# Performance work log

Measured on AMD Instinct MI355X. Metric: run time of the kernel, lower is better.

## Reference

```python
import jax, jax.numpy as jnp
import numpy as np

HIDDEN = 1024
N_HEAD = 16
HEAD_DIM = HIDDEN // N_HEAD
ROPE_THETA = 10000.0


def setup_inputs() -> dict:
    key = jax.random.key(0)
    ks = jax.random.split(key, 6)
    B, T = 4, 2048
    x = jax.random.normal(ks[0], (B, T, HIDDEN), dtype=jnp.float32)
    rnn_state = jax.random.normal(ks[1], (B, HIDDEN), dtype=jnp.float32)
    Wqkv = jax.random.normal(ks[2], (HIDDEN, 3 * HIDDEN), dtype=jnp.float32) * 0.02
    bqkv = jnp.zeros((3 * HIDDEN,), dtype=jnp.float32)
    Wproj = jax.random.normal(ks[3], (HIDDEN, HIDDEN), dtype=jnp.float32) * 0.02
    bproj = jnp.zeros((HIDDEN,), dtype=jnp.float32)
    return {"x": x, "rnn_state": rnn_state, "Wqkv": Wqkv, "bqkv": bqkv,
            "Wproj": Wproj, "bproj": bproj}


def _rope_tables(T, dtype):
    # GPT-NeoX style half-split RoPE
    inv_freq = 1.0 / (ROPE_THETA ** (jnp.arange(0, HEAD_DIM, 2, dtype=jnp.float32) / HEAD_DIM))
    freqs = jnp.arange(T, dtype=jnp.float32)[:, None] * inv_freq[None, :]  # [T, D/2]
    return jnp.cos(freqs).astype(dtype), jnp.sin(freqs).astype(dtype)


def _apply_rope(x, cos, sin):
    # x: [B, H, T, D]; cos/sin: [T, D/2]
    x1, x2 = jnp.split(x, 2, axis=-1)
    c = cos[None, None, :, :]
    s = sin[None, None, :, :]
    return jnp.concatenate([x1 * c - x2 * s, x1 * s + x2 * c], axis=-1)


def reference(x, rnn_state, Wqkv, bqkv, Wproj, bproj):
    B, T, C = x.shape
    qkv = x @ Wqkv + bqkv  # [B, T, 3C]
    q, k, v = jnp.split(qkv, 3, axis=-1)
    # split heads -> [B, H, T, D]
    def heads(t):
        return t.reshape(B, T, N_HEAD, HEAD_DIM).transpose(0, 2, 1, 3)
    q, k, v = heads(q), heads(k), heads(v)
    cos, sin = _rope_tables(T, x.dtype)
    q = _apply_rope(q, cos, sin)
    k = _apply_rope(k, cos, sin)
    scale = 1.0 / jnp.sqrt(jnp.asarray(HEAD_DIM, dtype=x.dtype))
    scores = jnp.einsum('bhtd,bhsd->bhts', q, k) * scale  # [B,H,T,T]
    # causal additive mask: 0 on/below diag, -inf above (matches torch buffer)
    causal = jnp.tril(jnp.ones((T, T), dtype=bool))
    scores = jnp.where(causal[None, None, :, :], scores, -jnp.inf)
    attn = jax.nn.softmax(scores, axis=-1)
    out = jnp.einsum('bhts,bhsd->bhtd', attn, v)  # [B,H,T,D]
    out = out.transpose(0, 2, 1, 3).reshape(B, T, C)
    output = out @ Wproj + bproj
    return (output, rnn_state)
```

## Files before the change

### kernel.cpp

```cpp
#include <hip/hip_runtime.h>
#include <cstdint>
#include <cstddef>
#include <math.h>

typedef unsigned short u16;
typedef __attribute__((ext_vector_type(8))) short short8;
typedef __attribute__((ext_vector_type(4))) float floatx4;

#define HIDDEN 1024
#define NHEAD 16
#define HD 64
#define BB 4
#define TT 2048
#define MM (BB*TT)
#define NQKV 3072
#define NEGINF (-30000.0f)

__device__ inline u16 f2bf(float f){
  union { float f; unsigned u; } v; v.f = f;
  unsigned r = v.u + 0x7FFFu + ((v.u >> 16) & 1u);
  return (u16)(r >> 16);
}
__device__ inline void load_lds16(const void* g, void* l){
  __builtin_amdgcn_global_load_lds((const __attribute__((address_space(1))) void*)g,
                                   (__attribute__((address_space(3))) void*)l,
                                   16, 0, 0);
}
__device__ inline short8 cvt8(const float* p){
  const floatx4 a = *(const floatx4*)p;
  const floatx4 b = *(const floatx4*)(p + 4);
  union { short8 s; unsigned u[4]; } r;
  asm("v_cvt_pk_bf16_f32 %0, %1, %2" : "=v"(r.u[0]) : "v"(a[0]), "v"(a[1]));
  asm("v_cvt_pk_bf16_f32 %0, %1, %2" : "=v"(r.u[1]) : "v"(a[2]), "v"(a[3]));
  asm("v_cvt_pk_bf16_f32 %0, %1, %2" : "=v"(r.u[2]) : "v"(b[0]), "v"(b[1]));
  asm("v_cvt_pk_bf16_f32 %0, %1, %2" : "=v"(r.u[3]) : "v"(b[2]), "v"(b[3]));
  return r.s;
}

#define PREP_CONV_BLKS  4096
#define PREP_TQKV_BLKS  (96*32)
#define PREP_TPROJ_BLKS (32*32)
#define PREP_ROPE_BLKS  (TT*32/256)
#define PREP_TAIL_BLKS  ((BB*HIDDEN+255)/256)
#define PREP_BLKS (PREP_CONV_BLKS + PREP_TQKV_BLKS + PREP_TPROJ_BLKS + PREP_ROPE_BLKS + PREP_TAIL_BLKS)

__global__ void prep(const float* __restrict__ x, u16* __restrict__ xN,
                     const float* __restrict__ Wqkv, u16* __restrict__ WqkvT,
                     const float* __restrict__ Wproj, u16* __restrict__ WprojT,
                     float* __restrict__ ropeC, float* __restrict__ ropeS,
                     const float* __restrict__ rnn, float* __restrict__ out)
{
  __shared__ alignas(16) u16 tile[32][33];
  int blk = blockIdx.x;
  const int tid = threadIdx.x;

  if (blk < PREP_CONV_BLKS){
    const int i = (blk * 256 + tid) * 8;
    #pragma unroll
    for (int u = 0; u < 8; u++) xN[i + u] = f2bf(x[i + u]);
    return;
  }
  blk -= PREP_CONV_BLKS;
  if (blk < PREP_TQKV_BLKS + PREP_TPROJ_BLKS){
    const float* in; u16* outp; int R, C, c0, r0;
    if (blk < PREP_TQKV_BLKS){
      in = Wqkv; outp = WqkvT; R = HIDDEN; C = NQKV;
      c0 = (blk % 96) * 32; r0 = (blk / 96) * 32;
    } else {
      const int b2 = blk - PREP_TQKV_BLKS;
      in = Wproj; outp = WprojT; R = HIDDEN; C = HIDDEN;
      c0 = (b2 % 32) * 32; r0 = (b2 / 32) * 32;
    }
    const int tx = tid & 31, ty = tid >> 5;
    for (int i = ty; i < 32; i += 8)
      tile[i][tx] = f2bf(in[(size_t)(r0 + i) * C + c0 + tx]);
    __syncthreads();
    for (int i = ty; i < 32; i += 8) outp[(size_t)(c0 + i) * R + r0 + tx] = tile[tx][i];
    return;
  }
  blk -= PREP_TQKV_BLKS + PREP_TPROJ_BLKS;
  if (blk < PREP_ROPE_BLKS){
    const int idx = blk * 256 + tid;
    const int t = idx >> 5, f = idx & 31;
    const float inv = powf(10000.0f, -(float)f * (1.0f / 32.0f));
    const float ang = (float)t * inv;
    ropeC[idx] = cosf(ang);
    ropeS[idx] = sinf(ang);
    return;
  }
  blk -= PREP_ROPE_BLKS;
  {
    const int i = blk * 256 + tid;
    if (i < BB * HIDDEN) out[(size_t)MM * HIDDEN + i] = rnn[i];
  }
}

__global__ void gemm_qkv(const u16* __restrict__ X, const u16* __restrict__ WT,
                         const float* __restrict__ bias,
                         const float* __restrict__ ropeC, const float* __restrict__ ropeS,
                         u16* __restrict__ Qb, u16* __restrict__ Kb, u16* __restrict__ Vtg)
{
  __shared__ alignas(16) u16 SB[8192];
  u16* const As = SB;
  u16* const Bs = SB + 4096;
  const int tid = threadIdx.x;
  const int wid = tid >> 6, lane = tid & 63;
  const int quad = lane >> 4, ln = lane & 15;
  const int row0 = blockIdx.y * 128, col0 = blockIdx.x * 128;
  const int wm = (wid >> 1) * 64, wn = (wid & 1) * 64;
  floatx4 acc[4][4] = {};

  const int sr = tid >> 2, sk = (tid & 3) * 8;

  for (int kk = 0; kk < 32; ++kk){
    const int k0 = kk * 32;
    __syncthreads();
    load_lds16(&X [(size_t)(row0 + sr      ) * 1024 + k0 + sk], &As[(size_t)(tid      ) * 8]);
    load_lds16(&X [(size_t)(row0 + sr + 64 ) * 1024 + k0 + sk], &As[(size_t)(tid + 256) * 8]);
    load_lds16(&WT[(size_t)(col0 + sr      ) * 1024 + k0 + sk], &Bs[(size_t)(tid      ) * 8]);
    load_lds16(&WT[(size_t)(col0 + sr + 64 ) * 1024 + k0 + sk], &Bs[(size_t)(tid + 256) * 8]);
    __syncthreads();
    short8 a[4], b[4];
    #pragma unroll
    for (int i = 0; i < 4; i++) a[i] = *(const short8*)&As[(wm + i*16 + ln) * 32 + quad * 8];
    #pragma unroll
    for (int j = 0; j < 4; j++) b[j] = *(const short8*)&Bs[(wn + j*16 + ln) * 32 + quad * 8];
    #pragma unroll
    for (int i = 0; i < 4; i++)
      #pragma unroll
      for (int j = 0; j < 4; j++)
        acc[i][j] = __builtin_amdgcn_mfma_f32_16x16x32_bf16(a[i], b[j], acc[i][j], 0, 0, 0);
  }

  __syncthreads();

  const int wcol0 = col0 + wn;
  const int which = wcol0 >> 10;
  const int h = (wcol0 & 1023) >> 6;
  float bs[4];
  #pragma unroll
  for (int j = 0; j < 4; j++) bs[j] = bias[wcol0 + j*16 + ln];

  if (which < 2){
    #pragma unroll
    for (int i = 0; i < 4; i++){
      #pragma unroll
      for (int rr = 0; rr < 4; rr++){
        const int rowg = row0 + wm + i*16 + quad*4 + rr;
        const int b_ = rowg >> 11, t = rowg & 2047;
        u16* op = (which == 0 ? Qb : Kb) + ((size_t)(b_ * NHEAD + h) * TT + t) * HD;
        #pragma unroll
        for (int j = 0; j < 2; j++){
          const int f = j*16 + ln;
          const float cs = ropeC[t * 32 + f];
          const float sn = ropeS[t * 32 + f];
          const float x1 = acc[i][j  ][rr] + bs[j  ];
          const float x2 = acc[i][j+2][rr] + bs[j+2];
          float y1 = x1 * cs - x2 * sn;
          float y2 = x1 * sn + x2 * cs;
          if (which == 0){ y1 *= 0.125f; y2 *= 0.125f; }
          op[f]      = f2bf(y1);
          op[f + 32] = f2bf(y2);
        }
      }
    }
  } else {
    u16* const vtx = SB + (size_t)wid * (64 * 24);
    #pragma unroll
    for (int i = 0; i < 4; i++){
      #pragma unroll
      for (int j = 0; j < 4; j++)
        #pragma unroll
        for (int rr = 0; rr < 4; rr++)
          vtx[(j*16 + ln) * 24 + quad*4 + rr] = f2bf(acc[i][j][rr] + bs[j]);
      asm volatile("s_waitcnt lgkmcnt(0)" ::: "memory");
      const int d = lane;
      const short8 v0 = *(const short8*)&vtx[d * 24 + 0];
      const short8 v1 = *(const short8*)&vtx[d * 24 + 8];
      const int rowg = row0 + wm + i*16;
      const int b_ = rowg >> 11, t0 = rowg & 2047;
      u16* vp = &Vtg[((size_t)(b_ * NHEAD + h) * HD + d) * TT + t0];
      *(short8*)&vp[0] = v0;
      *(short8*)&vp[8] = v1;
      asm volatile("s_waitcnt lgkmcnt(0)" ::: "memory");
    }
  }
}

__global__ void __launch_bounds__(256, 3)
attn(const u16* __restrict__ Qb, const u16* __restrict__ Kb,
     const u16* __restrict__ Vtg, u16* __restrict__ AO)
{
  const int bh = blockIdx.x, tbi = 15 - (int)blockIdx.y;
  const int tid = threadIdx.x;
  const int wid = tid >> 6, lane = tid & 63;
  const int quad = lane >> 4, ln = lane & 15;

  __shared__ alignas(16) u16 Kl2[2][64 * 72];
  __shared__ alignas(16) u16 Vt2[2][64 * 72];
  __shared__ alignas(16) float Plf[4][16 * 68];

  const u16* Qh = Qb  + (size_t)bh * TT * HD;
  const u16* Kh = Kb  + (size_t)bh * TT * HD;
  const u16* Vh = Vtg + (size_t)bh * HD * TT;
  const int b_ = bh >> 4, h = bh & 15;

  const int qbase = tbi * 128 + wid * 32;

  short8 aq[2][2];
  #pragma unroll
  for (int qt = 0; qt < 2; qt++){
    aq[qt][0] = *(const short8*)&Qh[(size_t)(qbase + qt*16 + ln) * HD + quad*8];
    aq[qt][1] = *(const short8*)&Qh[(size_t)(qbase + qt*16 + ln) * HD + 32 + quad*8];
  }

  floatx4 o[2][4] = {};
  float l_i[2][4] = {};
  float* Pf = &Plf[wid][0];

  const int pr = tid >> 3, pc = (tid & 7) * 8;
  short8 kpre0, kpre1, vpre0, vpre1;

  const int nch = 2 * (tbi + 1);

  kpre0 = *(const short8*)&Kh[(size_t)(pr     ) * HD + pc];
  kpre1 = *(const short8*)&Kh[(size_t)(pr + 32) * HD + pc];
  vpre0 = *(const short8*)&Vh[(size_t)(pr     ) * TT + pc];
  vpre1 = *(const short8*)&Vh[(size_t)(pr + 32) * TT + pc];
  *(short8*)&Kl2[0][(pr     ) * 72 + pc] = kpre0;
  *(short8*)&Kl2[0][(pr + 32) * 72 + pc] = kpre1;
  *(short8*)&Vt2[0][(pr     ) * 72 + pc] = vpre0;
  *(short8*)&Vt2[0][(pr + 32) * 72 + pc] = vpre1;
  __syncthreads();

  int cur = 0;
  for (int ch = 0; ch < nch; ++ch){
    const int key0 = ch * 64;
    if (ch + 1 < nch){
      const int nk0 = key0 + 64;
      kpre0 = *(const short8*)&Kh[(size_t)(nk0 + pr     ) * HD + pc];
      kpre1 = *(const short8*)&Kh[(size_t)(nk0 + pr + 32) * HD + pc];
      vpre0 = *(const short8*)&Vh[(size_t)(pr     ) * TT + nk0 + pc];
      vpre1 = *(const short8*)&Vh[(size_t)(pr + 32) * TT + nk0 + pc];
    }

    if (key0 <= qbase + 31){
      const u16* Kl = Kl2[cur];
      const u16* Vt = Vt2[cur];
      const bool act0 = (key0 <= qbase + 15);
      short8 pk0[2], pk1[2];
      #pragma unroll
      for (int qt = 0; qt < 2; qt++){
        if (qt == 0 && !act0) continue;
        const int qt0 = qbase + qt*16;
        floatx4 z[4];
        #pragma unroll
        for (int j = 0; j < 4; j++){
          const short8 kb0 = *(const short8*)&Kl[(j*16 + ln) * 72 + quad*8];
          const short8 kb1 = *(const short8*)&Kl[(j*16 + ln) * 72 + 32 + quad*8];
          floatx4 zz = {0.0f, 0.0f, 0.0f, 0.0f};
          zz = __builtin_amdgcn_mfma_f32_16x16x32_bf16(aq[qt][0], kb0, zz, 0, 0, 0);
          zz = __builtin_amdgcn_mfma_f32_16x16x32_bf16(aq[qt][1], kb1, zz, 0, 0, 0);
          z[j] = zz;
        }
        if (key0 + 63 > qt0){
          #pragma unroll
          for (int j = 0; j < 4; j++)
            #pragma unroll
            for (int rr = 0; rr < 4; rr++){
              const int key = key0 + j*16 + ln;
              const int t   = qt0 + quad*4 + rr;
              if (key > t) z[j][rr] = NEGINF;
            }
        }
        #pragma unroll
        for (int j = 0; j < 4; j++)
          #pragma unroll
          for (int rr = 0; rr < 4; rr++){
            const float p = __expf(z[j][rr]);
            l_i[qt][rr] += p;
            Pf[(quad*4 + rr) * 68 + j*16 + ln] = p;
          }
        asm volatile("s_waitcnt lgkmcnt(0)" ::: "memory");
        pk0[qt] = cvt8(&Pf[ln * 68 + quad*8]);
        pk1[qt] = cvt8(&Pf[ln * 68 + 32 + quad*8]);
      }
      #pragma unroll
      for (int n = 0; n < 4; n++){
        const short8 vb0 = *(const short8*)&Vt[(n*16 + ln) * 72 + quad*8];
        const short8 vb1 = *(const short8*)&Vt[(n*16 + ln) * 72 + 32 + quad*8];
        if (act0){
          o[0][n] = __builtin_amdgcn_mfma_f32_16x16x32_bf16(pk0[0], vb0, o[0][n], 0, 0, 0);
          o[0][n] = __builtin_amdgcn_mfma_f32_16x16x32_bf16(pk1[0], vb1, o[0][n], 0, 0, 0);
        }
        o[1][n] = __builtin_amdgcn_mfma_f32_16x16x32_bf16(pk0[1], vb0, o[1][n], 0, 0, 0);
        o[1][n] = __builtin_amdgcn_mfma_f32_16x16x32_bf16(pk1[1], vb1, o[1][n], 0, 0, 0);
      }
    }

    if (ch + 1 < nch){
      *(short8*)&Kl2[cur ^ 1][(pr     ) * 72 + pc] = kpre0;
      *(short8*)&Kl2[cur ^ 1][(pr + 32) * 72 + pc] = kpre1;
      *(short8*)&Vt2[cur ^ 1][(pr     ) * 72 + pc] = vpre0;
      *(short8*)&Vt2[cur ^ 1][(pr + 32) * 72 + pc] = vpre1;
    }
    __syncthreads();
    cur ^= 1;
  }

  #pragma unroll
  for (int qt = 0; qt < 2; qt++)
    #pragma unroll
    for (int rr = 0; rr < 4; rr++){
      float rs = l_i[qt][rr];
      #pragma unroll
      for (int off = 1; off < 16; off <<= 1) rs += __shfl_xor(rs, off);
      l_i[qt][rr] = rs;
    }

  #pragma unroll
  for (int qt = 0; qt < 2; qt++)
    #pragma unroll
    for (int n = 0; n < 4; n++)
      #pragma unroll
      for (int rr = 0; rr < 4; rr++){
        const int t = qbase + qt*16 + quad*4 + rr;
        const float inv_l = 1.0f / fmaxf(l_i[qt][rr], 1e-20f);
        AO[(size_t)(b_ * TT + t) * HIDDEN + h * HD + n*16 + ln] = f2bf(o[qt][n][rr] * inv_l);
      }
}

__global__ void gemm_proj(const u16* __restrict__ A, const u16* __restrict__ WT,
                          const float* __restrict__ bias, float* __restrict__ out)
{
  __shared__ alignas(16) u16 As[128 * 32];
  __shared__ alignas(16) u16 Bs[128 * 32];
  const int tid = threadIdx.x;
  const int wid = tid >> 6, lane = tid & 63;
  const int quad = lane >> 4, ln = lane & 15;
  const int row0 = blockIdx.y * 128, col0 = blockIdx.x * 128;
  const int wm = (wid >> 1) * 64, wn = (wid & 1) * 64;
  floatx4 acc[4][4] = {};

  const int sr = tid >> 2, sk = (tid & 3) * 8;

  for (int kk = 0; kk < 32; ++kk){
    const int k0 = kk * 32;
    __syncthreads();
    load_lds16(&A [(size_t)(row0 + sr      ) * 1024 + k0 + sk], &As[(size_t)(tid      ) * 8]);
    load_lds16(&A [(size_t)(row0 + sr + 64 ) * 1024 + k0 + sk], &As[(size_t)(tid + 256) * 8]);
    load_lds16(&WT[(size_t)(col0 + sr      ) * 1024 + k0 + sk], &Bs[(size_t)(tid      ) * 8]);
    load_lds16(&WT[(size_t)(col0 + sr + 64 ) * 1024 + k0 + sk], &Bs[(size_t)(tid + 256) * 8]);
    __syncthreads();
    short8 a[4], b[4];
    #pragma unroll
    for (int i = 0; i < 4; i++) a[i] = *(const short8*)&As[(wm + i*16 + ln) * 32 + quad * 8];
    #pragma unroll
    for (int j = 0; j < 4; j++) b[j] = *(const short8*)&Bs[(wn + j*16 + ln) * 32 + quad * 8];
    #pragma unroll
    for (int i = 0; i < 4; i++)
      #pragma unroll
      for (int j = 0; j < 4; j++)
        acc[i][j] = __builtin_amdgcn_mfma_f32_16x16x32_bf16(a[i], b[j], acc[i][j], 0, 0, 0);
  }

  float bs[4];
  #pragma unroll
  for (int j = 0; j < 4; j++) bs[j] = bias[col0 + wn + j*16 + ln];
  #pragma unroll
  for (int i = 0; i < 4; i++)
    #pragma unroll
    for (int rr = 0; rr < 4; rr++){
      const int rowg = row0 + wm + i*16 + quad*4 + rr;
      #pragma unroll
      for (int j = 0; j < 4; j++)
        out[(size_t)rowg * HIDDEN + col0 + wn + j*16 + ln] = acc[i][j][rr] + bs[j];
    }
}

extern "C" void kernel_launch(void* const* d_in, const int* in_sizes, int n_in,
                              void* d_out, int out_size, void* d_ws, size_t ws_size,
                              hipStream_t stream)
{
  const float* x     = (const float*)d_in[0];
  const float* rnn   = (const float*)d_in[1];
  const float* Wqkv  = (const float*)d_in[2];
  const float* bqkv  = (const float*)d_in[3];
  const float* Wproj = (const float*)d_in[4];
  const float* bproj = (const float*)d_in[5];
  float* out = (float*)d_out;

  char* ws = (char*)d_ws;
  size_t off = 0;
  float* ropeC  = (float*)(ws + off); off += (size_t)TT * 32 * 4;
  float* ropeS  = (float*)(ws + off); off += (size_t)TT * 32 * 4;
  u16*   xN     = (u16*)(ws + off);   off += (size_t)MM * HIDDEN * 2;
  u16*   WqkvT  = (u16*)(ws + off);   off += (size_t)NQKV * HIDDEN * 2;
  u16*   WprojT = (u16*)(ws + off);   off += (size_t)HIDDEN * HIDDEN * 2;
  u16*   Qb     = (u16*)(ws + off);   off += (size_t)MM * HIDDEN * 2;
  u16*   Kb     = (u16*)(ws + off);   off += (size_t)MM * HIDDEN * 2;
  u16*   Vtg    = (u16*)(ws + off);   off += (size_t)MM * HIDDEN * 2;
  u16*   AO     = (u16*)(ws + off);   off += (size_t)MM * HIDDEN * 2;

  prep<<<PREP_BLKS, 256, 0, stream>>>(x, xN, Wqkv, WqkvT, Wproj, WprojT,
                                      ropeC, ropeS, rnn, out);
  gemm_qkv<<<dim3(NQKV / 128, MM / 128), 256, 0, stream>>>(xN, WqkvT, bqkv, ropeC, ropeS, Qb, Kb, Vtg);
  attn<<<dim3(BB * NHEAD, 16), 256, 0, stream>>>(Qb, Kb, Vtg, AO);
  gemm_proj<<<dim3(HIDDEN / 128, MM / 128), 256, 0, stream>>>(AO, WprojT, bproj, out);
}
```

Before: 266.5 us.

## Pair light and heavy causal query tiles per attention block to balance work

Each attention block now handles two query tiles, a late one (tbi 15-y) and an early one (tbi y), so every block does the same total causal work. The grid shrinks from 16 to 8 tiles per head. K/V chunks staged in shared memory are reused by both tiles, which cuts global K/V reads. In exchange each thread holds twice the Q fragments and accumulators, so register pressure rises and occupancy under launch_bounds(256,3) may drop, and the grid falls to 512 blocks.

```diff
diff --git a/kernel.cpp b/kernel.cpp
--- a/kernel.cpp
+++ b/kernel.cpp
@@ -191,7 +191,9 @@
 attn(const u16* __restrict__ Qb, const u16* __restrict__ Kb,
      const u16* __restrict__ Vtg, u16* __restrict__ AO)
 {
-  const int bh = blockIdx.x, tbi = 15 - (int)blockIdx.y;
+  const int bh = blockIdx.x;
+  const int tbiL = (int)blockIdx.y;
+  const int tbiH = 15 - tbiL;
   const int tid = threadIdx.x;
   const int wid = tid >> 6, lane = tid & 63;
   const int quad = lane >> 4, ln = lane & 15;
@@ -205,23 +207,24 @@
   const u16* Vh = Vtg + (size_t)bh * HD * TT;
   const int b_ = bh >> 4, h = bh & 15;
 
-  const int qbase = tbi * 128 + wid * 32;
-
-  short8 aq[2][2];
-  #pragma unroll
-  for (int qt = 0; qt < 2; qt++){
-    aq[qt][0] = *(const short8*)&Qh[(size_t)(qbase + qt*16 + ln) * HD + quad*8];
-    aq[qt][1] = *(const short8*)&Qh[(size_t)(qbase + qt*16 + ln) * HD + 32 + quad*8];
-  }
-
-  floatx4 o[2][4] = {};
-  float l_i[2][4] = {};
+  const int qbase[2] = { tbiH * 128 + wid * 32, tbiL * 128 + wid * 32 };
+  const int nch[2]   = { 2 * (tbiH + 1), 2 * (tbiL + 1) };
+
+  short8 aq[2][2][2];
+  #pragma unroll
+  for (int tg = 0; tg < 2; tg++)
+    #pragma unroll
+    for (int qt = 0; qt < 2; qt++){
+      aq[tg][qt][0] = *(const short8*)&Qh[(size_t)(qbase[tg] + qt*16 + ln) * HD + quad*8];
+      aq[tg][qt][1] = *(const short8*)&Qh[(size_t)(qbase[tg] + qt*16 + ln) * HD + 32 + quad*8];
+    }
+
+  floatx4 o[2][2][4] = {};
+  float l_i[2][2][4] = {};
   float* Pf = &Plf[wid][0];
 
   const int pr = tid >> 3, pc = (tid & 7) * 8;
   short8 kpre0, kpre1, vpre0, vpre1;
-
-  const int nch = 2 * (tbi + 1);
 
   kpre0 = *(const short8*)&Kh[(size_t)(pr     ) * HD + pc];
   kpre1 = *(const short8*)&Kh[(size_t)(pr + 32) * HD + pc];
@@ -234,9 +237,9 @@
   __syncthreads();
 
   int cur = 0;
-  for (int ch = 0; ch < nch; ++ch){
+  for (int ch = 0; ch < nch[0]; ++ch){
     const int key0 = ch * 64;
-    if (ch + 1 < nch){
+    if (ch + 1 < nch[0]){
       const int nk0 = key0 + 64;
       kpre0 = *(const short8*)&Kh[(size_t)(nk0 + pr     ) * HD + pc];
       kpre1 = *(const short8*)&Kh[(size_t)(nk0 + pr + 32) * HD + pc];
@@ -244,23 +247,28 @@
       vpre1 = *(const short8*)&Vh[(size_t)(pr + 32) * TT + nk0 + pc];
     }
 
-    if (key0 <= qbase + 31){
-      const u16* Kl = Kl2[cur];
-      const u16* Vt = Vt2[cur];
-      const bool act0 = (key0 <= qbase + 15);
+    const u16* Kl = Kl2[cur];
+    const u16* Vt = Vt2[cur];
+
+    #pragma unroll
+    for (int tg = 0; tg < 2; tg++){
+      if (tg == 1 && ch >= nch[1]) continue;
+      const int qb = qbase[tg];
+      if (key0 > qb + 31) continue;
+      const bool act0 = (key0 <= qb + 15);
       short8 pk0[2], pk1[2];
       #pragma unroll
       for (int qt = 0; qt < 2; qt++){
         if (qt == 0 && !act0) continue;
-        const int qt0 = qbase + qt*16;
+        const int qt0 = qb + qt*16;
         floatx4 z[4];
         #pragma unroll
         for (int j = 0; j < 4; j++){
           const short8 kb0 = *(const short8*)&Kl[(j*16 + ln) * 72 + quad*8];
           const short8 kb1 = *(const short8*)&Kl[(j*16 + ln) * 72 + 32 + quad*8];
           floatx4 zz = {0.0f, 0.0f, 0.0f, 0.0f};
-          zz = __builtin_amdgcn_mfma_f32_16x16x32_bf16(aq[qt][0], kb0, zz, 0, 0, 0);
-          zz = __builtin_amdgcn_mfma_f32_16x16x32_bf16(aq[qt][1], kb1, zz, 0, 0, 0);
+          zz = __builtin_amdgcn_mfma_f32_16x16x32_bf16(aq[tg][qt][0], kb0, zz, 0, 0, 0);
+          zz = __builtin_amdgcn_mfma_f32_16x16x32_bf16(aq[tg][qt][1], kb1, zz, 0, 0, 0);
           z[j] = zz;
         }
         if (key0 + 63 > qt0){
@@ -278,7 +286,7 @@
           #pragma unroll
           for (int rr = 0; rr < 4; rr++){
             const float p = __expf(z[j][rr]);
-            l_i[qt][rr] += p;
+            l_i[tg][qt][rr] += p;
             Pf[(quad*4 + rr) * 68 + j*16 + ln] = p;
           }
         asm volatile("s_waitcnt lgkmcnt(0)" ::: "memory");
@@ -290,15 +298,15 @@
         const short8 vb0 = *(const short8*)&Vt[(n*16 + ln) * 72 + quad*8];
         const short8 vb1 = *(const short8*)&Vt[(n*16 + ln) * 72 + 32 + quad*8];
         if (act0){
-          o[0][n] = __builtin_amdgcn_mfma_f32_16x16x32_bf16(pk0[0], vb0, o[0][n], 0, 0, 0);
-          o[0][n] = __builtin_amdgcn_mfma_f32_16x16x32_bf16(pk1[0], vb1, o[0][n], 0, 0, 0);
+          o[tg][0][n] = __builtin_amdgcn_mfma_f32_16x16x32_bf16(pk0[0], vb0, o[tg][0][n], 0, 0, 0);
+          o[tg][0][n] = __builtin_amdgcn_mfma_f32_16x16x32_bf16(pk1[0], vb1, o[tg][0][n], 0, 0, 0);
         }
-        o[1][n] = __builtin_amdgcn_mfma_f32_16x16x32_bf16(pk0[1], vb0, o[1][n], 0, 0, 0);
-        o[1][n] = __builtin_amdgcn_mfma_f32_16x16x32_bf16(pk1[1], vb1, o[1][n], 0, 0, 0);
+        o[tg][1][n] = __builtin_amdgcn_mfma_f32_16x16x32_bf16(pk0[1], vb0, o[tg][1][n], 0, 0, 0);
+        o[tg][1][n] = __builtin_amdgcn_mfma_f32_16x16x32_bf16(pk1[1], vb1, o[tg][1][n], 0, 0, 0);
       }
     }
 
-    if (ch + 1 < nch){
+    if (ch + 1 < nch[0]){
       *(short8*)&Kl2[cur ^ 1][(pr     ) * 72 + pc] = kpre0;
       *(short8*)&Kl2[cur ^ 1][(pr + 32) * 72 + pc] = kpre1;
       *(short8*)&Vt2[cur ^ 1][(pr     ) * 72 + pc] = vpre0;
@@ -309,25 +317,29 @@
   }
 
   #pragma unroll
-  for (int qt = 0; qt < 2; qt++)
-    #pragma unroll
-    for (int rr = 0; rr < 4; rr++){
-      float rs = l_i[qt][rr];
-      #pragma unroll
-      for (int off = 1; off < 16; off <<= 1) rs += __shfl_xor(rs, off);
-      l_i[qt][rr] = rs;
-    }
-
-  #pragma unroll
-  for (int qt = 0; qt < 2; qt++)
-    #pragma unroll
-    for (int n = 0; n < 4; n++)
+  for (int tg = 0; tg < 2; tg++)
+    #pragma unroll
+    for (int qt = 0; qt < 2; qt++)
       #pragma unroll
       for (int rr = 0; rr < 4; rr++){
-        const int t = qbase + qt*16 + quad*4 + rr;
-        const float inv_l = 1.0f / fmaxf(l_i[qt][rr], 1e-20f);
-        AO[(size_t)(b_ * TT + t) * HIDDEN + h * HD + n*16 + ln] = f2bf(o[qt][n][rr] * inv_l);
+        float rs = l_i[tg][qt][rr];
+        #pragma unroll
+        for (int off = 1; off < 16; off <<= 1) rs += __shfl_xor(rs, off);
+        l_i[tg][qt][rr] = rs;
       }
+
+  #pragma unroll
+  for (int tg = 0; tg < 2; tg++)
+    #pragma unroll
+    for (int qt = 0; qt < 2; qt++)
+      #pragma unroll
+      for (int n = 0; n < 4; n++)
+        #pragma unroll
+        for (int rr = 0; rr < 4; rr++){
+          const int t = qbase[tg] + qt*16 + quad*4 + rr;
+          const float inv_l = 1.0f / fmaxf(l_i[tg][qt][rr], 1e-20f);
+          AO[(size_t)(b_ * TT + t) * HIDDEN + h * HD + n*16 + ln] = f2bf(o[tg][qt][n][rr] * inv_l);
+        }
 }
 
 __global__ void gemm_proj(const u16* __restrict__ A, const u16* __restrict__ WT,
@@ -405,6 +417,6 @@
   prep<<<PREP_BLKS, 256, 0, stream>>>(x, xN, Wqkv, WqkvT, Wproj, WprojT,
                                       ropeC, ropeS, rnn, out);
   gemm_qkv<<<dim3(NQKV / 128, MM / 128), 256, 0, stream>>>(xN, WqkvT, bqkv, ropeC, ropeS, Qb, Kb, Vtg);
-  attn<<<dim3(BB * NHEAD, 16), 256, 0, stream>>>(Qb, Kb, Vtg, AO);
+  attn<<<dim3(BB * NHEAD, 8), 256, 0, stream>>>(Qb, Kb, Vtg, AO);
   gemm_proj<<<dim3(HIDDEN / 128, MM / 128), 256, 0, stream>>>(AO, WprojT, bproj, out);
 }
```

Result: slower. 304.5 us (+14.3%).
